# Performance work log

Measured on AMD Instinct MI355X. Metric: run time of the kernel, lower is better.

## Reference

```python
import math
import jax, jax.numpy as jnp
import numpy as np

BS, Q_LEN, DIM = 8, 16, 4096
MAX_SEQ = 4096
N_Q_HEADS, N_KV_HEADS, HEAD_DIM = 32, 8, 128
REP = N_Q_HEADS // N_KV_HEADS


def setup_inputs() -> dict:
    key = jax.random.key(0)
    ks = jax.random.split(key, 12)
    w = 0.02
    return {
        "x": jax.random.normal(ks[0], (BS, Q_LEN, DIM), jnp.float32),
        "k_cache": jax.random.normal(ks[1], (BS, MAX_SEQ, N_KV_HEADS, HEAD_DIM), jnp.float32),
        "v_cache": jax.random.normal(ks[2], (BS, MAX_SEQ, N_KV_HEADS, HEAD_DIM), jnp.float32),
        "Wq": jax.random.normal(ks[3], (DIM, N_Q_HEADS * HEAD_DIM), jnp.float32) * w,
        "bq": jax.random.normal(ks[4], (N_Q_HEADS * HEAD_DIM,), jnp.float32) * w,
        "Wk": jax.random.normal(ks[5], (DIM, N_KV_HEADS * HEAD_DIM), jnp.float32) * w,
        "bk": jax.random.normal(ks[6], (N_KV_HEADS * HEAD_DIM,), jnp.float32) * w,
        "Wv": jax.random.normal(ks[7], (DIM, N_KV_HEADS * HEAD_DIM), jnp.float32) * w,
        "bv": jax.random.normal(ks[8], (N_KV_HEADS * HEAD_DIM,), jnp.float32) * w,
        "Wo": jax.random.normal(ks[9], (N_Q_HEADS * HEAD_DIM, DIM), jnp.float32) * w,
        "bo": jax.random.normal(ks[10], (DIM,), jnp.float32) * w,
        "start_pos": MAX_SEQ - Q_LEN,
        "seq_len_for_kv": Q_LEN,
    }


def reference(x, k_cache, v_cache, Wq, bq, Wk, bk, Wv, bv, Wo, bo, start_pos, seq_len_for_kv):
    bs, sl, dim = x.shape
    # Projections (torch Linear: x @ W^T + b; here W stored as [in, out])
    q = (x @ Wq + bq).reshape(bs, sl, N_KV_HEADS, REP, HEAD_DIM)  # [b, q, g, r, d]
    k = (x @ Wk + bk).reshape(bs, sl, N_KV_HEADS, HEAD_DIM)
    v = (x @ Wv + bv).reshape(bs, sl, N_KV_HEADS, HEAD_DIM)
    # KV-cache append (start_pos / seq_len_for_kv are static Python ints)
    k_cache = k_cache.at[:, start_pos:start_pos + seq_len_for_kv].set(k)
    v_cache = v_cache.at[:, start_pos:start_pos + seq_len_for_kv].set(v)
    kv_len = start_pos + seq_len_for_kv
    keys = k_cache[:, :kv_len]    # [b, L, g, d]
    vals = v_cache[:, :kv_len]    # [b, L, g, d]
    # GQA: each kv head g serves REP query heads r (broadcast instead of repeat_kv)
    scale = 1.0 / math.sqrt(HEAD_DIM)
    scores = jnp.einsum('bqgrd,blgd->bgrql', q, keys) * scale  # [b, g, r, q, L]
    att = jax.nn.softmax(scores, axis=-1)
    out = jnp.einsum('bgrql,blgd->bqgrd', att, vals)           # [b, q, g, r, d]
    out = out.reshape(bs, sl, N_Q_HEADS * HEAD_DIM)
    return out @ Wo + bo
```

## Files before the change

### kernel.cpp

```cpp
#include <hip/hip_runtime.h>
#include <math.h>

#define DIM       4096
#define NKVH      8
#define HD        128
#define MAX_SEQ   4096
#define START_POS 4080
#define NQKV      6144
#define NCHUNK    8
#define CHUNK     512
#define KS        8
#define ATT_SCALE 0.08838834764831845f

#define WS_PART   0
#define WS_QH     6291456
#define WS_QL     6553600
#define WS_KNEW   6815744
#define WS_VNEW   6946816
#define WS_PM     7077888
#define WS_PL     7110656
#define WS_ATH    7143424
#define WS_ATL    7405568
#define WS_XH     7667712
#define WS_XL     7929856
#define WS_PARTO  WS_PART

typedef __bf16 bf16x8 __attribute__((ext_vector_type(8)));
typedef float  f32x4  __attribute__((ext_vector_type(4)));
typedef unsigned int uintx4 __attribute__((ext_vector_type(4)));

__device__ __forceinline__ unsigned short f2bf(float f) {
    union { float f; unsigned int u; } v; v.f = f;
    unsigned int r = v.u + 0x7FFFu + ((v.u >> 16) & 1u);
    return (unsigned short)(r >> 16);
}
__device__ __forceinline__ float bf2f(unsigned short h) {
    union { unsigned int u; float f; } v; v.u = ((unsigned int)h) << 16;
    return v.f;
}
__device__ __forceinline__ void splitbf(float f, unsigned short &h, unsigned short &l) {
    h = f2bf(f);
    l = f2bf(f - bf2f(h));
}
__device__ __forceinline__ bf16x8 ldsfrag(const unsigned short* p) {
    uintx4 u = *(const uintx4*)p;
    return __builtin_bit_cast(bf16x8, u);
}
__device__ __forceinline__ bf16x8 ldsfrag2(const unsigned short* p) {
    union { uint2 u2[2]; bf16x8 v; } u;
    u.u2[0] = *(const uint2*)p;
    u.u2[1] = *(const uint2*)(p + 4);
    return u.v;
}
#define MFMA16(a,b,c) __builtin_amdgcn_mfma_f32_16x16x32_bf16(a, b, c, 0, 0, 0)
#define VCOMP(v,j) ((j)==0?(v).x:((j)==1?(v).y:((j)==2?(v).z:(v).w)))

__global__ __launch_bounds__(256) void split_x_kernel(
    const float* __restrict__ x, unsigned short* __restrict__ xh,
    unsigned short* __restrict__ xl, int n)
{
    int i = blockIdx.x * 256 + threadIdx.x;
    if (i < n) { unsigned short h, l; splitbf(x[i], h, l); xh[i] = h; xl[i] = l; }
}

__device__ __forceinline__ void gemm_body(
    const unsigned short* __restrict__ Ah, const unsigned short* __restrict__ Al,
    const float* __restrict__ W, int ldW, int noff,
    float* __restrict__ part, int partStride, int ncol0, int ks,
    unsigned short* Ahs, unsigned short* Als, unsigned short* Bs)
{
    const int t = threadIdx.x;
    const int w = t >> 6, lane = t & 63, l15 = lane & 15, quad = lane >> 4;
    f32x4 acc[2][4];
    #pragma unroll
    for (int i = 0; i < 2; ++i)
        #pragma unroll
        for (int nt = 0; nt < 4; ++nt) acc[i][nt] = (f32x4){0.f, 0.f, 0.f, 0.f};

    const int k0base = ks * 512;
    uintx4 areg_h[4], areg_l[4];
    float4 wreg[4];

    auto LOAD = [&](int it) {
        int k0 = k0base + it * 64;
        #pragma unroll
        for (int i = 0; i < 4; ++i) {
            int f = t + i * 256;
            int row = f >> 3, c0 = (f & 7) << 3;
            size_t off = (size_t)row * DIM + k0 + c0;
            areg_h[i] = *(const uintx4*)(Ah + off);
            areg_l[i] = *(const uintx4*)(Al + off);
        }
        #pragma unroll
        for (int i = 0; i < 4; ++i) {
            int kk = (t >> 4) + 16 * i;
            int n0 = (t & 15) << 2;
            wreg[i] = *(const float4*)(W + (size_t)(k0 + kk) * ldW + noff + n0);
        }
    };

    LOAD(0);
    for (int it = 0; it < 8; ++it) {
        __syncthreads();
        #pragma unroll
        for (int i = 0; i < 4; ++i) {
            int f = t + i * 256;
            int row = f >> 3, c0 = (f & 7) << 3;
            *(uintx4*)(Ahs + row * 72 + c0) = areg_h[i];
            *(uintx4*)(Als + row * 72 + c0) = areg_l[i];
        }
        {
            int n0 = (t & 15) << 2;
            #pragma unroll
            for (int i = 0; i < 4; ++i) {
                int kk = (t >> 4) + 16 * i;
                #pragma unroll
                for (int j = 0; j < 4; ++j)
                    Bs[(n0 + j) * 68 + kk] = f2bf(VCOMP(wreg[i], j));
            }
        }
        __syncthreads();
        if (it < 7) LOAD(it + 1);
        #pragma unroll
        for (int kt = 0; kt < 2; ++kt) {
            int ko = kt * 32 + quad * 8;
            bf16x8 ah0 = ldsfrag(Ahs + ((2*w+0)*16 + l15) * 72 + ko);
            bf16x8 ah1 = ldsfrag(Ahs + ((2*w+1)*16 + l15) * 72 + ko);
            bf16x8 al0 = ldsfrag(Als + ((2*w+0)*16 + l15) * 72 + ko);
            bf16x8 al1 = ldsfrag(Als + ((2*w+1)*16 + l15) * 72 + ko);
            #pragma unroll
            for (int nt = 0; nt < 4; ++nt) {
                bf16x8 b = ldsfrag2(Bs + (nt*16 + l15) * 68 + ko);
                acc[0][nt] = MFMA16(ah0, b, acc[0][nt]);
                acc[0][nt] = MFMA16(al0, b, acc[0][nt]);
                acc[1][nt] = MFMA16(ah1, b, acc[1][nt]);
                acc[1][nt] = MFMA16(al1, b, acc[1][nt]);
            }
        }
    }
    #pragma unroll
    for (int i = 0; i < 2; ++i)
        #pragma unroll
        for (int nt = 0; nt < 4; ++nt)
            #pragma unroll
            for (int r = 0; r < 4; ++r) {
                int row = (2*w + i) * 16 + quad * 4 + r;
                int col = ncol0 + nt * 16 + l15;
                part[(size_t)(ks * 128 + row) * partStride + col] = acc[i][nt][r];
            }
}

__global__ __launch_bounds__(256) void qkv_gemm_kernel(
    const unsigned short* __restrict__ xh, const unsigned short* __restrict__ xl,
    const float* __restrict__ Wq, const float* __restrict__ Wk,
    const float* __restrict__ Wv, float* __restrict__ part)
{
    __shared__ unsigned short Ahs[128 * 72], Als[128 * 72];
    __shared__ unsigned short Bs[64 * 68];
    int ncol0 = blockIdx.x * 64;
    int ks = blockIdx.y;
    const float* W; int ldW, noff;
    if (ncol0 < 4096)      { W = Wq; ldW = 4096; noff = ncol0; }
    else if (ncol0 < 5120) { W = Wk; ldW = 1024; noff = ncol0 - 4096; }
    else                   { W = Wv; ldW = 1024; noff = ncol0 - 5120; }
    gemm_body(xh, xl, W, ldW, noff, part, NQKV, ncol0, ks, Ahs, Als, Bs);
}

__global__ __launch_bounds__(256) void oproj_gemm_kernel(
    const unsigned short* __restrict__ ah, const unsigned short* __restrict__ al,
    const float* __restrict__ Wo, float* __restrict__ part)
{
    __shared__ unsigned short Ahs[128 * 72], Als[128 * 72];
    __shared__ unsigned short Bs[64 * 68];
    int ncol0 = blockIdx.x * 64;
    int ks = blockIdx.y;
    gemm_body(ah, al, Wo, 4096, ncol0, part, 4096, ncol0, ks, Ahs, Als, Bs);
}

__global__ __launch_bounds__(256) void qkv_reduce_kernel(
    const float* __restrict__ part, const float* __restrict__ bq,
    const float* __restrict__ bk, const float* __restrict__ bv,
    unsigned short* __restrict__ qh, unsigned short* __restrict__ ql,
    float* __restrict__ k_new, float* __restrict__ v_new)
{
    int gid = blockIdx.x * 256 + threadIdx.x;
    int row = gid / NQKV;
    int n   = gid - row * NQKV;
    float s = 0.f;
    #pragma unroll
    for (int j = 0; j < KS; ++j)
        s += part[(size_t)(j * 128 + row) * NQKV + n];
    if (n < 4096) {
        float v = s + bq[n];
        unsigned short h, l; splitbf(v, h, l);
        qh[row * 4096 + n] = h; ql[row * 4096 + n] = l;
    } else if (n < 5120) k_new[row * 1024 + (n - 4096)] = s + bk[n - 4096];
    else                 v_new[row * 1024 + (n - 5120)] = s + bv[n - 5120];
}

__global__ __launch_bounds__(256) void attn_partial3_kernel(
    const unsigned short* __restrict__ qhp, const unsigned short* __restrict__ qlp,
    const float* __restrict__ kc, const float* __restrict__ vc,
    const float* __restrict__ knew, const float* __restrict__ vnew,
    float* __restrict__ part_O, float* __restrict__ part_m, float* __restrict__ part_l)
{
    __shared__ unsigned short Kb[32 * 136];
    __shared__ unsigned short Vt[128 * 36];
    __shared__ unsigned short Pw[4 * 16 * 36];
    const int t = threadIdx.x;
    const int w = t >> 6, lane = t & 63, l15 = lane & 15, quad = lane >> 4;
    const int blk = blockIdx.x;
    const int b = blk >> 6, g = (blk >> 3) & 7, c = blk & 7;

    bf16x8 qhf[4], qlf[4];
    {
        size_t base = (size_t)(b * 16 + l15) * DIM + (g * 4 + w) * HD + quad * 8;
        #pragma unroll
        for (int kt = 0; kt < 4; ++kt) {
            qhf[kt] = ldsfrag(qhp + base + kt * 32);
            qlf[kt] = ldsfrag(qlp + base + kt * 32);
        }
    }

    float m_run[4], l_run[4];
    f32x4 oacc[8];
    #pragma unroll
    for (int r = 0; r < 4; ++r) { m_run[r] = -INFINITY; l_run[r] = 0.f; }
    #pragma unroll
    for (int d = 0; d < 8; ++d) oacc[d] = (f32x4){0.f, 0.f, 0.f, 0.f};

    float4 kreg[4], vreg[4];
    auto LOADKV = [&](int it) {
        #pragma unroll
        for (int i = 0; i < 4; ++i) {
            int f = t + i * 256;
            int pos = f >> 5, d0 = (f & 31) << 2;
            int pg = c * CHUNK + it * 32 + pos;
            const float *ksrc, *vsrc;
            if (pg >= START_POS) {
                size_t off = (size_t)(b * 16 + pg - START_POS) * (NKVH * HD) + g * HD + d0;
                ksrc = knew + off; vsrc = vnew + off;
            } else {
                size_t off = ((size_t)(b * MAX_SEQ + pg) * NKVH + g) * HD + d0;
                ksrc = kc + off; vsrc = vc + off;
            }
            kreg[i] = *(const float4*)ksrc;
            vreg[i] = *(const float4*)vsrc;
        }
    };

    unsigned short* phw = Pw + w * 576;

    LOADKV(0);
    for (int it = 0; it < CHUNK / 32; ++it) {
        __syncthreads();
        #pragma unroll
        for (int i = 0; i < 4; ++i) {
            int f = t + i * 256;
            int pos = f >> 5, d0 = (f & 31) << 2;
            ushort4 k4 = make_ushort4(f2bf(kreg[i].x), f2bf(kreg[i].y),
                                      f2bf(kreg[i].z), f2bf(kreg[i].w));
            *(ushort4*)&Kb[pos * 136 + d0] = k4;
        }
        {
            int p0 = t >> 5, d0 = (t & 31) << 2;
            #pragma unroll
            for (int j = 0; j < 4; ++j) {
                ushort4 v4 = make_ushort4(f2bf(VCOMP(vreg[0], j)), f2bf(VCOMP(vreg[1], j)),
                                          f2bf(VCOMP(vreg[2], j)), f2bf(VCOMP(vreg[3], j)));
                *(ushort4*)&Vt[(d0 + j) * 36 + p0 * 4] = v4;
            }
        }
        __syncthreads();
        if (it + 1 < CHUNK / 32) LOADKV(it + 1);

        f32x4 sacc[2];
        sacc[0] = (f32x4){0.f,0.f,0.f,0.f};
        sacc[1] = (f32x4){0.f,0.f,0.f,0.f};
        #pragma unroll
        for (int nt = 0; nt < 2; ++nt)
            #pragma unroll
            for (int kt = 0; kt < 4; ++kt) {
                bf16x8 bh = ldsfrag(&Kb[(nt*16 + l15) * 136 + kt*32 + quad*8]);
                sacc[nt] = MFMA16(qhf[kt], bh, sacc[nt]);
                sacc[nt] = MFMA16(qlf[kt], bh, sacc[nt]);
            }

        float e0[4], e1[4], alpha[4];
        #pragma unroll
        for (int r = 0; r < 4; ++r) {
            float s0 = sacc[0][r] * ATT_SCALE;
            float s1 = sacc[1][r] * ATT_SCALE;
            float mx = fmaxf(s0, s1);
            mx = fmaxf(mx, __shfl_xor(mx, 1));
            mx = fmaxf(mx, __shfl_xor(mx, 2));
            mx = fmaxf(mx, __shfl_xor(mx, 4));
            mx = fmaxf(mx, __shfl_xor(mx, 8));
            float mnew = fmaxf(m_run[r], mx);
            alpha[r] = __expf(m_run[r] - mnew);
            e0[r] = __expf(s0 - mnew);
            e1[r] = __expf(s1 - mnew);
            float sum = e0[r] + e1[r];
            sum += __shfl_xor(sum, 1);
            sum += __shfl_xor(sum, 2);
            sum += __shfl_xor(sum, 4);
            sum += __shfl_xor(sum, 8);
            l_run[r] = l_run[r] * alpha[r] + sum;
            m_run[r] = mnew;
        }
        #pragma unroll
        for (int d = 0; d < 8; ++d)
            #pragma unroll
            for (int r = 0; r < 4; ++r) oacc[d][r] *= alpha[r];

        {
            int slot0 = 4 * (l15 & 7) + (l15 >> 3);
            #pragma unroll
            for (int r = 0; r < 4; ++r) {
                phw[(quad*4 + r) * 36 + slot0]     = f2bf(e0[r]);
                phw[(quad*4 + r) * 36 + slot0 + 2] = f2bf(e1[r]);
            }
        }
        bf16x8 pa = ldsfrag(phw + l15 * 36 + quad * 8);

        #pragma unroll
        for (int dt = 0; dt < 8; ++dt) {
            bf16x8 vb = ldsfrag(&Vt[(dt*16 + l15) * 36 + quad * 8]);
            oacc[dt] = MFMA16(pa, vb, oacc[dt]);
        }
    }

    #pragma unroll
    for (int dt = 0; dt < 8; ++dt)
        #pragma unroll
        for (int r = 0; r < 4; ++r)
            part_O[((size_t)blk * 64 + w * 16 + quad * 4 + r) * HD + dt * 16 + l15] = oacc[dt][r];
    if (l15 == 0) {
        #pragma unroll
        for (int r = 0; r < 4; ++r) {
            part_m[blk * 64 + w * 16 + quad * 4 + r] = m_run[r];
            part_l[blk * 64 + w * 16 + quad * 4 + r] = l_run[r];
        }
    }
}

__global__ __launch_bounds__(128) void attn_combine_kernel(
    const float* __restrict__ part_O, const float* __restrict__ part_m,
    const float* __restrict__ part_l, unsigned short* __restrict__ ah,
    unsigned short* __restrict__ al)
{
    int bid = blockIdx.x;
    int d = threadIdx.x;
    int bg = bid >> 6;
    int row = bid & 63;
    float mc[NCHUNK], lc[NCHUNK];
    float M = -INFINITY;
    #pragma unroll
    for (int cc = 0; cc < NCHUNK; ++cc) {
        mc[cc] = part_m[(bg * NCHUNK + cc) * 64 + row];
        lc[cc] = part_l[(bg * NCHUNK + cc) * 64 + row];
        M = fmaxf(M, mc[cc]);
    }
    float L = 0.f, acc = 0.f;
    #pragma unroll
    for (int cc = 0; cc < NCHUNK; ++cc) {
        float wgt = __expf(mc[cc] - M);
        L += lc[cc] * wgt;
        acc += part_O[((size_t)(bg * NCHUNK + cc) * 64 + row) * HD + d] * wgt;
    }
    int b = bg >> 3, g = bg & 7;
    int r = row >> 4, qp = row & 15;
    float v = acc / L;
    unsigned short h, l; splitbf(v, h, l);
    size_t idx = (size_t)(b * 16 + qp) * DIM + (g * 4 + r) * HD + d;
    ah[idx] = h; al[idx] = l;
}

__global__ __launch_bounds__(256) void oproj_reduce_kernel(
    const float* __restrict__ part, const float* __restrict__ bo,
    float* __restrict__ out)
{
    int gid = blockIdx.x * 256 + threadIdx.x;
    int n = gid & 4095;
    float s = 0.f;
    #pragma unroll
    for (int j = 0; j < KS; ++j) s += part[(size_t)j * 524288 + gid];
    out[gid] = s + bo[n];
}

extern "C" void kernel_launch(void* const* d_in, const int* in_sizes, int n_in,
                              void* d_out, int out_size, void* d_ws, size_t ws_size,
                              hipStream_t stream)
{
    const float* x  = (const float*)d_in[0];
    const float* kc = (const float*)d_in[1];
    const float* vc = (const float*)d_in[2];
    const float* Wq = (const float*)d_in[3];
    const float* bq = (const float*)d_in[4];
    const float* Wk = (const float*)d_in[5];
    const float* bk = (const float*)d_in[6];
    const float* Wv = (const float*)d_in[7];
    const float* bv = (const float*)d_in[8];
    const float* Wo = (const float*)d_in[9];
    const float* bo = (const float*)d_in[10];
    float* out = (float*)d_out;
    float* ws  = (float*)d_ws;

    unsigned short* xh = (unsigned short*)(ws + WS_XH);
    unsigned short* xl = (unsigned short*)(ws + WS_XL);
    unsigned short* qh = (unsigned short*)(ws + WS_QH);
    unsigned short* ql = (unsigned short*)(ws + WS_QL);
    unsigned short* ath = (unsigned short*)(ws + WS_ATH);
    unsigned short* atl = (unsigned short*)(ws + WS_ATL);

    split_x_kernel<<<2048, 256, 0, stream>>>(x, xh, xl, 524288);
    qkv_gemm_kernel<<<dim3(96, KS), 256, 0, stream>>>(xh, xl, Wq, Wk, Wv, ws + WS_PART);
    qkv_reduce_kernel<<<3072, 256, 0, stream>>>(ws + WS_PART, bq, bk, bv,
                                                qh, ql, ws + WS_KNEW, ws + WS_VNEW);
    attn_partial3_kernel<<<512, 256, 0, stream>>>(qh, ql, kc, vc,
                                                  ws + WS_KNEW, ws + WS_VNEW,
                                                  ws + WS_PARTO, ws + WS_PM, ws + WS_PL);
    attn_combine_kernel<<<4096, 128, 0, stream>>>(ws + WS_PARTO, ws + WS_PM,
                                                  ws + WS_PL, ath, atl);
    oproj_gemm_kernel<<<dim3(64, KS), 256, 0, stream>>>(ath, atl, Wo, ws + WS_PART);
    oproj_reduce_kernel<<<2048, 256, 0, stream>>>(ws + WS_PART, bo, out);
}
```

Baseline: 435.3 us.

## Split each attention chunk across two wave groups with in-block softmax merge

The attention partial kernel now launches 512 threads per block. Two groups of four waves each process half of the 512-position chunk, using separate shared-memory K/V tiles, and their online-softmax states are merged through shared memory before the result is written. This doubles the waves in flight to hide the latency of streaming the fp32 KV cache, at the cost of more shared memory, an extra merge step and tighter register limits. The bf16 conversion is also switched from manual rounding to the compiler's native conversion.

```diff
diff --git a/kernel.cpp b/kernel.cpp
--- a/kernel.cpp
+++ b/kernel.cpp
@@ -30,9 +30,7 @@
 typedef unsigned int uintx4 __attribute__((ext_vector_type(4)));
 
 __device__ __forceinline__ unsigned short f2bf(float f) {
-    union { float f; unsigned int u; } v; v.f = f;
-    unsigned int r = v.u + 0x7FFFu + ((v.u >> 16) & 1u);
-    return (unsigned short)(r >> 16);
+    return __builtin_bit_cast(unsigned short, (__bf16)f);
 }
 __device__ __forceinline__ float bf2f(unsigned short h) {
     union { unsigned int u; float f; } v; v.u = ((unsigned int)h) << 16;
@@ -198,23 +196,32 @@
     else                 v_new[row * 1024 + (n - 5120)] = s + bv[n - 5120];
 }
 
-__global__ __launch_bounds__(256) void attn_partial3_kernel(
+__global__ __launch_bounds__(512, 4) void attn_partial3_kernel(
     const unsigned short* __restrict__ qhp, const unsigned short* __restrict__ qlp,
     const float* __restrict__ kc, const float* __restrict__ vc,
     const float* __restrict__ knew, const float* __restrict__ vnew,
     float* __restrict__ part_O, float* __restrict__ part_m, float* __restrict__ part_l)
 {
-    __shared__ unsigned short Kb[32 * 136];
-    __shared__ unsigned short Vt[128 * 36];
-    __shared__ unsigned short Pw[4 * 16 * 36];
+    __shared__ __align__(16) unsigned char smem[45056];
+    unsigned short* KbAll = (unsigned short*)smem;
+    unsigned short* VtAll = (unsigned short*)(smem + 17408);
+    unsigned short* PwAll = (unsigned short*)(smem + 35840);
+
     const int t = threadIdx.x;
     const int w = t >> 6, lane = t & 63, l15 = lane & 15, quad = lane >> 4;
+    const int h = w >> 2;
+    const int rep = w & 3;
+    const int tl = t & 255;
     const int blk = blockIdx.x;
     const int b = blk >> 6, g = (blk >> 3) & 7, c = blk & 7;
 
+    unsigned short* Kbh = KbAll + h * (32 * 136);
+    unsigned short* Vth = VtAll + h * (128 * 36);
+    unsigned short* phw = PwAll + w * 576;
+
     bf16x8 qhf[4], qlf[4];
     {
-        size_t base = (size_t)(b * 16 + l15) * DIM + (g * 4 + w) * HD + quad * 8;
+        size_t base = (size_t)(b * 16 + l15) * DIM + (g * 4 + rep) * HD + quad * 8;
         #pragma unroll
         for (int kt = 0; kt < 4; ++kt) {
             qhf[kt] = ldsfrag(qhp + base + kt * 32);
@@ -233,9 +240,9 @@
     auto LOADKV = [&](int it) {
         #pragma unroll
         for (int i = 0; i < 4; ++i) {
-            int f = t + i * 256;
+            int f = tl + i * 256;
             int pos = f >> 5, d0 = (f & 31) << 2;
-            int pg = c * CHUNK + it * 32 + pos;
+            int pg = c * CHUNK + h * 256 + it * 32 + pos;
             const float *ksrc, *vsrc;
             if (pg >= START_POS) {
                 size_t off = (size_t)(b * 16 + pg - START_POS) * (NKVH * HD) + g * HD + d0;
@@ -249,30 +256,28 @@
         }
     };
 
-    unsigned short* phw = Pw + w * 576;
-
     LOADKV(0);
-    for (int it = 0; it < CHUNK / 32; ++it) {
+    for (int it = 0; it < 8; ++it) {
         __syncthreads();
         #pragma unroll
         for (int i = 0; i < 4; ++i) {
-            int f = t + i * 256;
+            int f = tl + i * 256;
             int pos = f >> 5, d0 = (f & 31) << 2;
             ushort4 k4 = make_ushort4(f2bf(kreg[i].x), f2bf(kreg[i].y),
                                       f2bf(kreg[i].z), f2bf(kreg[i].w));
-            *(ushort4*)&Kb[pos * 136 + d0] = k4;
+            *(ushort4*)&Kbh[pos * 136 + d0] = k4;
         }
         {
-            int p0 = t >> 5, d0 = (t & 31) << 2;
+            int p0 = tl >> 5, d0 = (tl & 31) << 2;
             #pragma unroll
             for (int j = 0; j < 4; ++j) {
                 ushort4 v4 = make_ushort4(f2bf(VCOMP(vreg[0], j)), f2bf(VCOMP(vreg[1], j)),
                                           f2bf(VCOMP(vreg[2], j)), f2bf(VCOMP(vreg[3], j)));
-                *(ushort4*)&Vt[(d0 + j) * 36 + p0 * 4] = v4;
+                *(ushort4*)&Vth[(d0 + j) * 36 + p0 * 4] = v4;
             }
         }
         __syncthreads();
-        if (it + 1 < CHUNK / 32) LOADKV(it + 1);
+        if (it + 1 < 8) LOADKV(it + 1);
 
         f32x4 sacc[2];
         sacc[0] = (f32x4){0.f,0.f,0.f,0.f};
@@ -281,7 +286,7 @@
         for (int nt = 0; nt < 2; ++nt)
             #pragma unroll
             for (int kt = 0; kt < 4; ++kt) {
-                bf16x8 bh = ldsfrag(&Kb[(nt*16 + l15) * 136 + kt*32 + quad*8]);
+                bf16x8 bh = ldsfrag(&Kbh[(nt*16 + l15) * 136 + kt*32 + quad*8]);
                 sacc[nt] = MFMA16(qhf[kt], bh, sacc[nt]);
                 sacc[nt] = MFMA16(qlf[kt], bh, sacc[nt]);
             }
@@ -325,22 +330,56 @@
 
         #pragma unroll
         for (int dt = 0; dt < 8; ++dt) {
-            bf16x8 vb = ldsfrag(&Vt[(dt*16 + l15) * 36 + quad * 8]);
+            bf16x8 vb = ldsfrag(&Vth[(dt*16 + l15) * 36 + quad * 8]);
             oacc[dt] = MFMA16(pa, vb, oacc[dt]);
         }
     }
 
-    #pragma unroll
-    for (int dt = 0; dt < 8; ++dt)
-        #pragma unroll
-        for (int r = 0; r < 4; ++r)
-            part_O[((size_t)blk * 64 + w * 16 + quad * 4 + r) * HD + dt * 16 + l15] = oacc[dt][r];
-    if (l15 == 0) {
+    __syncthreads();
+    float* mO = (float*)smem;
+    float* mm = (float*)(smem + 33792);
+    float* ml = (float*)(smem + 34048);
+    if (h == 1) {
+        #pragma unroll
+        for (int dt = 0; dt < 8; ++dt)
+            #pragma unroll
+            for (int r = 0; r < 4; ++r)
+                mO[(rep*16 + quad*4 + r) * 132 + dt*16 + l15] = oacc[dt][r];
+        if (l15 == 0)
+            #pragma unroll
+            for (int r = 0; r < 4; ++r) {
+                mm[rep*16 + quad*4 + r] = m_run[r];
+                ml[rep*16 + quad*4 + r] = l_run[r];
+            }
+    }
+    __syncthreads();
+    if (h == 0) {
+        float alpha[4], beta[4];
         #pragma unroll
         for (int r = 0; r < 4; ++r) {
-            part_m[blk * 64 + w * 16 + quad * 4 + r] = m_run[r];
-            part_l[blk * 64 + w * 16 + quad * 4 + r] = l_run[r];
-        }
+            int row = rep*16 + quad*4 + r;
+            float mB = mm[row], lB = ml[row];
+            float M = fmaxf(m_run[r], mB);
+            alpha[r] = __expf(m_run[r] - M);
+            beta[r]  = __expf(mB - M);
+            l_run[r] = l_run[r] * alpha[r] + lB * beta[r];
+            m_run[r] = M;
+        }
+        #pragma unroll
+        for (int dt = 0; dt < 8; ++dt)
+            #pragma unroll
+            for (int r = 0; r < 4; ++r) {
+                int row = rep*16 + quad*4 + r;
+                float ob = mO[row * 132 + dt*16 + l15];
+                part_O[((size_t)blk * 64 + row) * HD + dt*16 + l15] =
+                    oacc[dt][r] * alpha[r] + ob * beta[r];
+            }
+        if (l15 == 0)
+            #pragma unroll
+            for (int r = 0; r < 4; ++r) {
+                part_m[blk * 64 + rep*16 + quad*4 + r] = m_run[r];
+                part_l[blk * 64 + rep*16 + quad*4 + r] = l_run[r];
+            }
     }
 }
 
@@ -417,7 +456,7 @@
     qkv_gemm_kernel<<<dim3(96, KS), 256, 0, stream>>>(xh, xl, Wq, Wk, Wv, ws + WS_PART);
     qkv_reduce_kernel<<<3072, 256, 0, stream>>>(ws + WS_PART, bq, bk, bv,
                                                 qh, ql, ws + WS_KNEW, ws + WS_VNEW);
-    attn_partial3_kernel<<<512, 256, 0, stream>>>(qh, ql, kc, vc,
+    attn_partial3_kernel<<<512, 512, 0, stream>>>(qh, ql, kc, vc,
                                                   ws + WS_KNEW, ws + WS_VNEW,
                                                   ws + WS_PARTO, ws + WS_PM, ws + WS_PL);
     attn_combine_kernel<<<4096, 128, 0, stream>>>(ws + WS_PARTO, ws + WS_PM,
```

New measurement: 454.5 us. +4.4%, slower.

## Process two KV heads per block with contiguous loads and two-stage register prefetch

Applied to the files above, without the earlier changes.

The attention partial kernel now uses 512-thread blocks, each covering two adjacent KV heads. Each KV-cache row segment it reads is 1 KB contiguous instead of 512 B, and the grid is halved to 256 blocks. KV loads are prefetched two iterations ahead into double-buffered registers, the V transpose buffer gets a wider pitch, and float-to-bf16 conversion uses the hardware __bf16 cast. The aim is better DRAM coalescing and more latency hiding on the memory-bound KV streaming. The cost is higher register pressure and fewer blocks across the GPU.

```diff
diff --git a/kernel.cpp b/kernel.cpp
--- a/kernel.cpp
+++ b/kernel.cpp
@@ -30,9 +30,7 @@
 typedef unsigned int uintx4 __attribute__((ext_vector_type(4)));
 
 __device__ __forceinline__ unsigned short f2bf(float f) {
-    union { float f; unsigned int u; } v; v.f = f;
-    unsigned int r = v.u + 0x7FFFu + ((v.u >> 16) & 1u);
-    return (unsigned short)(r >> 16);
+    return __builtin_bit_cast(unsigned short, (__bf16)f);
 }
 __device__ __forceinline__ float bf2f(unsigned short h) {
     union { unsigned int u; float f; } v; v.u = ((unsigned int)h) << 16;
@@ -198,23 +196,32 @@
     else                 v_new[row * 1024 + (n - 5120)] = s + bv[n - 5120];
 }
 
-__global__ __launch_bounds__(256) void attn_partial3_kernel(
+__global__ __launch_bounds__(512, 2) void attn_partial4_kernel(
     const unsigned short* __restrict__ qhp, const unsigned short* __restrict__ qlp,
     const float* __restrict__ kc, const float* __restrict__ vc,
     const float* __restrict__ knew, const float* __restrict__ vnew,
     float* __restrict__ part_O, float* __restrict__ part_m, float* __restrict__ part_l)
 {
-    __shared__ unsigned short Kb[32 * 136];
-    __shared__ unsigned short Vt[128 * 36];
-    __shared__ unsigned short Pw[4 * 16 * 36];
+    __shared__ unsigned short Kb[2][32][136];
+    __shared__ unsigned short Vt[2][128][44];
+    __shared__ unsigned short Pw[8][16 * 36];
+
     const int t = threadIdx.x;
     const int w = t >> 6, lane = t & 63, l15 = lane & 15, quad = lane >> 4;
+    const int gsel = w >> 2;
+    const int rep  = w & 3;
     const int blk = blockIdx.x;
-    const int b = blk >> 6, g = (blk >> 3) & 7, c = blk & 7;
+    const int b = blk >> 5, gg = (blk >> 3) & 3, c = blk & 7;
+    const int g = gg * 2 + gsel;
+
+    const int p0 = t >> 6;
+    const int q4 = t & 63;
+    const int gl = q4 >> 5;
+    const int d0 = (q4 & 31) << 2;
 
     bf16x8 qhf[4], qlf[4];
     {
-        size_t base = (size_t)(b * 16 + l15) * DIM + (g * 4 + w) * HD + quad * 8;
+        size_t base = (size_t)(b * 16 + l15) * DIM + (g * 4 + rep) * HD + quad * 8;
         #pragma unroll
         for (int kt = 0; kt < 4; ++kt) {
             qhf[kt] = ldsfrag(qhp + base + kt * 32);
@@ -229,50 +236,47 @@
     #pragma unroll
     for (int d = 0; d < 8; ++d) oacc[d] = (f32x4){0.f, 0.f, 0.f, 0.f};
 
-    float4 kreg[4], vreg[4];
-    auto LOADKV = [&](int it) {
+    float4 kreg[2][4], vreg[2][4];
+    auto LOADKV = [&](int buf, int it) {
         #pragma unroll
         for (int i = 0; i < 4; ++i) {
-            int f = t + i * 256;
-            int pos = f >> 5, d0 = (f & 31) << 2;
+            int pos = p0 + i * 8;
             int pg = c * CHUNK + it * 32 + pos;
             const float *ksrc, *vsrc;
             if (pg >= START_POS) {
-                size_t off = (size_t)(b * 16 + pg - START_POS) * (NKVH * HD) + g * HD + d0;
+                size_t off = (size_t)(b * 16 + pg - START_POS) * (NKVH * HD) + gg * 256 + q4 * 4;
                 ksrc = knew + off; vsrc = vnew + off;
             } else {
-                size_t off = ((size_t)(b * MAX_SEQ + pg) * NKVH + g) * HD + d0;
+                size_t off = ((size_t)(b * MAX_SEQ + pg) * NKVH) * HD + gg * 256 + q4 * 4;
                 ksrc = kc + off; vsrc = vc + off;
             }
-            kreg[i] = *(const float4*)ksrc;
-            vreg[i] = *(const float4*)vsrc;
+            kreg[buf][i] = *(const float4*)ksrc;
+            vreg[buf][i] = *(const float4*)vsrc;
         }
     };
 
-    unsigned short* phw = Pw + w * 576;
-
-    LOADKV(0);
-    for (int it = 0; it < CHUNK / 32; ++it) {
+    unsigned short* phw = Pw[w];
+
+    LOADKV(0, 0);
+    LOADKV(1, 1);
+    for (int it = 0; it < 16; ++it) {
+        const int buf = it & 1;
         __syncthreads();
         #pragma unroll
         for (int i = 0; i < 4; ++i) {
-            int f = t + i * 256;
-            int pos = f >> 5, d0 = (f & 31) << 2;
-            ushort4 k4 = make_ushort4(f2bf(kreg[i].x), f2bf(kreg[i].y),
-                                      f2bf(kreg[i].z), f2bf(kreg[i].w));
-            *(ushort4*)&Kb[pos * 136 + d0] = k4;
-        }
-        {
-            int p0 = t >> 5, d0 = (t & 31) << 2;
-            #pragma unroll
-            for (int j = 0; j < 4; ++j) {
-                ushort4 v4 = make_ushort4(f2bf(VCOMP(vreg[0], j)), f2bf(VCOMP(vreg[1], j)),
-                                          f2bf(VCOMP(vreg[2], j)), f2bf(VCOMP(vreg[3], j)));
-                *(ushort4*)&Vt[(d0 + j) * 36 + p0 * 4] = v4;
-            }
-        }
+            int pos = p0 + i * 8;
+            ushort4 k4 = make_ushort4(f2bf(kreg[buf][i].x), f2bf(kreg[buf][i].y),
+                                      f2bf(kreg[buf][i].z), f2bf(kreg[buf][i].w));
+            *(ushort4*)&Kb[gl][pos][d0] = k4;
+        }
+        #pragma unroll
+        for (int j = 0; j < 4; ++j) {
+            ushort4 v4 = make_ushort4(f2bf(VCOMP(vreg[buf][0], j)), f2bf(VCOMP(vreg[buf][1], j)),
+                                      f2bf(VCOMP(vreg[buf][2], j)), f2bf(VCOMP(vreg[buf][3], j)));
+            *(ushort4*)&Vt[gl][d0 + j][p0 * 4] = v4;
+        }
+        if (it + 2 < 16) LOADKV(buf, it + 2);
         __syncthreads();
-        if (it + 1 < CHUNK / 32) LOADKV(it + 1);
 
         f32x4 sacc[2];
         sacc[0] = (f32x4){0.f,0.f,0.f,0.f};
@@ -281,7 +285,7 @@
         for (int nt = 0; nt < 2; ++nt)
             #pragma unroll
             for (int kt = 0; kt < 4; ++kt) {
-                bf16x8 bh = ldsfrag(&Kb[(nt*16 + l15) * 136 + kt*32 + quad*8]);
+                bf16x8 bh = ldsfrag(&Kb[gsel][nt*16 + l15][kt*32 + quad*8]);
                 sacc[nt] = MFMA16(qhf[kt], bh, sacc[nt]);
                 sacc[nt] = MFMA16(qlf[kt], bh, sacc[nt]);
             }
@@ -325,21 +329,22 @@
 
         #pragma unroll
         for (int dt = 0; dt < 8; ++dt) {
-            bf16x8 vb = ldsfrag(&Vt[(dt*16 + l15) * 36 + quad * 8]);
+            bf16x8 vb = ldsfrag(&Vt[gsel][dt*16 + l15][quad * 8]);
             oacc[dt] = MFMA16(pa, vb, oacc[dt]);
         }
     }
 
+    const size_t obase = (size_t)((b * 8 + g) * 8 + c) * 64 + rep * 16 + quad * 4;
     #pragma unroll
     for (int dt = 0; dt < 8; ++dt)
         #pragma unroll
         for (int r = 0; r < 4; ++r)
-            part_O[((size_t)blk * 64 + w * 16 + quad * 4 + r) * HD + dt * 16 + l15] = oacc[dt][r];
+            part_O[(obase + r) * HD + dt * 16 + l15] = oacc[dt][r];
     if (l15 == 0) {
         #pragma unroll
         for (int r = 0; r < 4; ++r) {
-            part_m[blk * 64 + w * 16 + quad * 4 + r] = m_run[r];
-            part_l[blk * 64 + w * 16 + quad * 4 + r] = l_run[r];
+            part_m[obase + r] = m_run[r];
+            part_l[obase + r] = l_run[r];
         }
     }
 }
@@ -417,7 +422,7 @@
     qkv_gemm_kernel<<<dim3(96, KS), 256, 0, stream>>>(xh, xl, Wq, Wk, Wv, ws + WS_PART);
     qkv_reduce_kernel<<<3072, 256, 0, stream>>>(ws + WS_PART, bq, bk, bv,
                                                 qh, ql, ws + WS_KNEW, ws + WS_VNEW);
-    attn_partial3_kernel<<<512, 256, 0, stream>>>(qh, ql, kc, vc,
+    attn_partial4_kernel<<<256, 512, 0, stream>>>(qh, ql, kc, vc,
                                                   ws + WS_KNEW, ws + WS_VNEW,
                                                   ws + WS_PARTO, ws + WS_PM, ws + WS_PL);
     attn_combine_kernel<<<4096, 128, 0, stream>>>(ws + WS_PARTO, ws + WS_PM,
```

New measurement: 537.8 us. 23.6% more time.
